# Performance work log

Hardware: AMD Instinct MI355X
Metric: run time of the kernel (lower is better)

Reference implementation:

```python
import jax, jax.numpy as jnp
import numpy as np
from jax import lax

T, B, DX, H, DZ = 512, 64, 128, 256, 64
W_SCALE = 0.05


def setup_inputs() -> dict:
    key = jax.random.key(0)
    ks = jax.random.split(key, 16)
    r = lambda k, shape, s=W_SCALE: jax.random.normal(k, shape, dtype=jnp.float32) * s
    return {
        "X": jax.random.normal(ks[0], (T, B, DX), dtype=jnp.float32),
        "Wih_f": r(ks[1], (H, DX)), "Whh_f": r(ks[2], (H, H)),
        "bih_f": r(ks[3], (H,)), "bhh_f": r(ks[4], (H,)),
        "Wih_b": r(ks[5], (H, DX)), "Whh_b": r(ks[6], (H, H)),
        "bih_b": r(ks[7], (H,)), "bhh_b": r(ks[8], (H,)),
        "Wt": r(ks[9], (H, DZ)), "bt": r(ks[10], (H,)),
        "Wmu": r(ks[11], (DZ, H)), "bmu": r(ks[12], (DZ,)),
        "Wsig": r(ks[13], (DZ, H)), "bsig": r(ks[14], (DZ,)),
        "eps": jax.random.normal(ks[15], (T, B, DZ), dtype=jnp.float32),
    }


def _rnn_dir(X, Wih, Whh, bih, bhh):
    # Elman RNN (tanh): h_t = tanh(x_t Wih^T + bih + h_{t-1} Whh^T + bhh)
    xproj = jnp.einsum('tbd,hd->tbh', X, Wih) + bih + bhh  # big GEMM hoisted out of scan

    def step(h, xp):
        h = jnp.tanh(xp + h @ Whh.T)
        return h, h

    h0 = jnp.zeros((X.shape[1], Whh.shape[0]), dtype=X.dtype)
    _, hs = lax.scan(step, h0, xproj)
    return hs  # [T,B,H]


def reference(X, Wih_f, Whh_f, bih_f, bhh_f, Wih_b, Whh_b, bih_b, bhh_b,
              Wt, bt, Wmu, bmu, Wsig, bsig, eps):
    h_left = _rnn_dir(X, Wih_f, Whh_f, bih_f, bhh_f)
    h_right = _rnn_dir(X[::-1], Wih_b, Whh_b, bih_b, bhh_b)[::-1]

    def step(z_prev, inputs):
        hl, hr, eps_t = inputs
        tmp = jnp.tanh(z_prev @ Wt.T + bt)           # transition_net
        h_t = (tmp + hl + hr) * (1.0 / 3.0)
        mu = h_t @ Wmu.T + bmu
        std = jax.nn.softplus(h_t @ Wsig.T + bsig)
        z = mu + std * eps_t                         # reparameterization
        return z, (z, mu, std)

    z0 = jnp.zeros((X.shape[1], Wt.shape[1]), dtype=X.dtype)
    _, (z, mu, std) = lax.scan(step, z0, (h_left, h_right, eps))
    # stack outputs {z_post, mu_post, std_post} into one array [3,T,B,DZ]
    return jnp.stack([z, mu, std])
```

## Files before the change

kernel.cpp:

```cpp
#include <hip/hip_runtime.h>

#define TT 512
#define BB 64
#define DXX 128
#define HH 256
#define DZZ 64

typedef __attribute__((ext_vector_type(8))) short short8;
typedef __attribute__((ext_vector_type(4))) float f32x4;

#define DEV static __device__ __forceinline__
#define MFMA(a,b,c) __builtin_amdgcn_mfma_f32_16x16x32_bf16((a),(b),(c),0,0,0)

DEV unsigned short f2bf(float f){
  unsigned u = __builtin_bit_cast(unsigned, f);
  u += 0x7FFFu + ((u >> 16) & 1u);
  return (unsigned short)(u >> 16);
}
DEV unsigned pack2(float lo, float hi){
  return (unsigned)f2bf(lo) | ((unsigned)f2bf(hi) << 16);
}
DEV float bfLO(unsigned u){ return __builtin_bit_cast(float, u << 16); }
DEV float bfHI(unsigned u){ return __builtin_bit_cast(float, u & 0xffff0000u); }
DEV float ftanh(float x){
  float a = fabsf(x);
  float e = __expf(-2.f * a);
  float r = __builtin_amdgcn_rcpf(1.f + e);
  float t = (1.f - e) * r;
  return copysignf(t, x);
}
DEV float fsoftplus(float x){
  float e = __expf(fminf(x, 20.f));
  float s = __logf(1.f + e);
  return (x > 20.f) ? x : s;
}
DEV void barrier_l(){
  asm volatile("s_waitcnt lgkmcnt(0)\n\ts_barrier" ::: "memory");
}


__global__ __launch_bounds__(256, 2) void phaseA(
    const float* __restrict__ X,
    const float* __restrict__ WihF, const float* __restrict__ bihF, const float* __restrict__ bhhF,
    const float* __restrict__ WihB, const float* __restrict__ bihB, const float* __restrict__ bhhB,
    unsigned short* __restrict__ xpF)
{
  const int bid = blockIdx.x;
  const int d = bid >> 9, s = bid & 511;
  const int ts = d ? (TT - 1 - s) : s;
  const float* W  = d ? WihB : WihF;
  const float* bi = d ? bihB : bihF;
  const float* bh = d ? bhhB : bhhF;

  const int tid = threadIdx.x, q = tid >> 6, l = tid & 63;
  const int l15 = l & 15, l4 = l >> 4;

  short8 wf[4][4];
  f32x4 bias[4];
  #pragma unroll
  for (int ni = 0; ni < 4; ++ni){
    int n = 64*q + 16*ni + l15;
    #pragma unroll
    for (int ks = 0; ks < 4; ++ks){
      const float* p = W + (size_t)n * DXX + ks*32 + l4*8;
      short8 v;
      #pragma unroll
      for (int i = 0; i < 8; ++i) v[i] = (short)f2bf(p[i]);
      wf[ni][ks] = v;
    }
    int n0 = 64*q + 16*ni + 4*l4;
    float4 b1 = *(const float4*)(bi + n0);
    float4 b2 = *(const float4*)(bh + n0);
    bias[ni][0]=b1.x+b2.x; bias[ni][1]=b1.y+b2.y; bias[ni][2]=b1.z+b2.z; bias[ni][3]=b1.w+b2.w;
  }

  #pragma unroll
  for (int bq = 0; bq < 4; ++bq){
    const float* xr = X + ((size_t)ts * 64 + 16*bq + l15) * DXX;
    short8 xf[4];
    #pragma unroll
    for (int ks = 0; ks < 4; ++ks){
      const float* p = xr + ks*32 + l4*8;
      short8 v;
      #pragma unroll
      for (int i = 0; i < 8; ++i) v[i] = (short)f2bf(p[i]);
      xf[ks] = v;
    }

    f32x4 acc[4];
    #pragma unroll
    for (int ni = 0; ni < 4; ++ni) acc[ni] = MFMA(wf[ni][0], xf[0], bias[ni]);
    #pragma unroll
    for (int ks = 1; ks < 4; ++ks)
      #pragma unroll
      for (int ni = 0; ni < 4; ++ni)
        acc[ni] = MFMA(wf[ni][ks], xf[ks], acc[ni]);

    unsigned wd[8];
    #pragma unroll
    for (int ni = 0; ni < 4; ++ni){
      wd[ni*2]   = pack2(acc[ni][0], acc[ni][1]);
      wd[ni*2+1] = pack2(acc[ni][2], acc[ni][3]);
    }
    unsigned short* dst = xpF + ((((size_t)d*TT + s)*4 + bq)*4 + q)*1024 + (size_t)l*16;
    uint4 o0 = {wd[0], wd[1], wd[2], wd[3]};
    uint4 o1 = {wd[4], wd[5], wd[6], wd[7]};
    ((uint4*)dst)[0] = o0;
    ((uint4*)dst)[1] = o1;
  }
}

__global__ __launch_bounds__(256, 1) void phaseB(
    const float* __restrict__ WhhF, const float* __restrict__ WhhB,
    const unsigned short* __restrict__ xpF, unsigned short* __restrict__ hF)
{
  const int dir = blockIdx.x >> 2, bq = blockIdx.x & 3;
  const float* Whh = dir ? WhhB : WhhF;
  const int tid = threadIdx.x, q = tid >> 6, l = tid & 63;
  const int l15 = l & 15, l4 = l >> 4;
  const int swz = (l15 & 7) << 3;
  const int rbase = l15 * 256;

  __shared__ __attribute__((aligned(16))) unsigned short hbuf[2][4096];

  short8 wf[4][8];
  #pragma unroll
  for (int ni = 0; ni < 4; ++ni){
    int n = 64*q + 16*ni + l15;
    #pragma unroll
    for (int ks = 0; ks < 8; ++ks){
      const float* p = Whh + (size_t)n * HH + ks*32 + l4*8;
      short8 v;
      #pragma unroll
      for (int i = 0; i < 8; ++i) v[i] = (short)f2bf(p[i]);
      wf[ni][ks] = v;
    }
  }
  for (int i = tid; i < 2048; i += 256) ((unsigned*)hbuf[0])[i] = 0u;

  const size_t strideS = 16384;
  const size_t laneOff = (size_t)bq*4096 + (size_t)q*1024 + (size_t)l*16;
  const unsigned short* xpP = xpF + (size_t)dir*TT*strideS + laneOff;
  unsigned short* hD = hF + (size_t)dir*TT*strideS + laneOff;

  uint4 xqA0, xqA1, xqB0, xqB1;
  { const uint4* p = (const uint4*)xpP;             xqA0 = p[0]; xqA1 = p[1]; }
  { const uint4* p = (const uint4*)(xpP + strideS); xqB0 = p[0]; xqB1 = p[1]; }

  barrier_l();

  auto bstep = [&](int s, uint4& XQ0, uint4& XQ1,
                   const unsigned short* RD, unsigned short* WR){
    short8 b[8];
    #pragma unroll
    for (int ks = 0; ks < 8; ++ks)
      b[ks] = *(const short8*)(RD + ((rbase + ks*32 + l4*8) ^ swz));
    f32x4 accE[4], accO[4];
    {
      unsigned W8[8] = {XQ0.x, XQ0.y, XQ0.z, XQ0.w, XQ1.x, XQ1.y, XQ1.z, XQ1.w};
      #pragma unroll
      for (int ni = 0; ni < 4; ++ni){
        accE[ni][0] = bfLO(W8[ni*2]);   accE[ni][1] = bfHI(W8[ni*2]);
        accE[ni][2] = bfLO(W8[ni*2+1]); accE[ni][3] = bfHI(W8[ni*2+1]);
        accO[ni][0] = 0.f; accO[ni][1] = 0.f; accO[ni][2] = 0.f; accO[ni][3] = 0.f;
      }
    }
    {
      int sn = (s + 2 < TT) ? s + 2 : TT - 1;
      const uint4* src = (const uint4*)(xpP + (size_t)sn * strideS);
      XQ0 = src[0]; XQ1 = src[1];
    }
    #pragma unroll
    for (int ks = 0; ks < 8; ks += 2){
      #pragma unroll
      for (int ni = 0; ni < 4; ++ni){
        accE[ni] = MFMA(wf[ni][ks],   b[ks],   accE[ni]);
        accO[ni] = MFMA(wf[ni][ks+1], b[ks+1], accO[ni]);
      }
    }
    unsigned wd[8];
    #pragma unroll
    for (int ni = 0; ni < 4; ++ni){
      float t0 = ftanh(accE[ni][0] + accO[ni][0]);
      float t1 = ftanh(accE[ni][1] + accO[ni][1]);
      float t2 = ftanh(accE[ni][2] + accO[ni][2]);
      float t3 = ftanh(accE[ni][3] + accO[ni][3]);
      unsigned lo = pack2(t0, t1), hi = pack2(t2, t3);
      wd[ni*2] = lo; wd[ni*2+1] = hi;
      int ea = rbase + ((64*q + 16*ni + 4*l4) ^ swz);
      uint2 v; v.x = lo; v.y = hi;
      *(uint2*)(WR + ea) = v;
    }
    {
      size_t off = (size_t)(dir ? (TT - 1 - s) : s) * strideS;
      uint4 o0 = {wd[0], wd[1], wd[2], wd[3]};
      uint4 o1 = {wd[4], wd[5], wd[6], wd[7]};
      *(uint4*)(hD + off)     = o0;
      *(uint4*)(hD + off + 8) = o1;
    }
    barrier_l();
  };

  for (int s = 0; s < TT; s += 2){
    bstep(s,     xqA0, xqA1, hbuf[0], hbuf[1]);
    bstep(s + 1, xqB0, xqB1, hbuf[1], hbuf[0]);
  }
}

__global__ __launch_bounds__(256, 1) void phaseC(
    const float* __restrict__ Wt,  const float* __restrict__ bt,
    const float* __restrict__ Wmu, const float* __restrict__ bmu,
    const float* __restrict__ Wsig,const float* __restrict__ bsig,
    const float* __restrict__ eps, const unsigned short* __restrict__ hF,
    float* __restrict__ out)
{
  const int bq = blockIdx.x;
  const int tid = threadIdx.x, q = tid >> 6, l = tid & 63;
  const int l15 = l & 15, l4 = l >> 4;
  const int swz = (l15 & 7) << 3;
  const int rbase = l15 * 256;
  const int zrbase = l15 * 64;

  __shared__ __attribute__((aligned(16))) unsigned short zbuf[1024];
  __shared__ __attribute__((aligned(16))) unsigned short hbuf[4096];

  short8 wtf[4][2]; f32x4 btb[4];
  #pragma unroll
  for (int ni = 0; ni < 4; ++ni){
    int n = 64*q + 16*ni + l15;
    #pragma unroll
    for (int ks = 0; ks < 2; ++ks){
      const float* p = Wt + (size_t)n * DZZ + ks*32 + l4*8;
      short8 v;
      #pragma unroll
      for (int i = 0; i < 8; ++i) v[i] = (short)f2bf(p[i]);
      wtf[ni][ks] = v;
    }
    float4 b4 = *(const float4*)(bt + 64*q + 16*ni + 4*l4);
    btb[ni][0]=b4.x; btb[ni][1]=b4.y; btb[ni][2]=b4.z; btb[ni][3]=b4.w;
  }
  short8 wm[8], wsg[8];
  {
    int r = 16*q + l15;
    #pragma unroll
    for (int ks = 0; ks < 8; ++ks){
      const float* pm = Wmu  + (size_t)r * HH + ks*32 + l4*8;
      const float* ps = Wsig + (size_t)r * HH + ks*32 + l4*8;
      short8 vm, vs;
      #pragma unroll
      for (int i = 0; i < 8; ++i){ vm[i] = (short)f2bf(pm[i]); vs[i] = (short)f2bf(ps[i]); }
      wm[ks] = vm; wsg[ks] = vs;
    }
  }
  f32x4 bm4, bs4;
  {
    float4 a = *(const float4*)(bmu  + 16*q + 4*l4);
    float4 b = *(const float4*)(bsig + 16*q + 4*l4);
    bm4[0]=a.x; bm4[1]=a.y; bm4[2]=a.z; bm4[3]=a.w;
    bs4[0]=b.x; bs4[1]=b.y; bs4[2]=b.z; bs4[3]=b.w;
  }
  for (int i = tid; i < 512; i += 256) ((unsigned*)zbuf)[i] = 0u;

  const size_t strideS = 16384;
  const size_t laneOff = (size_t)bq*4096 + (size_t)q*1024 + (size_t)l*16;
  const unsigned short* hLp = hF + laneOff;
  const unsigned short* hRp = hLp + (size_t)TT * strideS;
  const float* eP = eps + ((size_t)(16*bq + l15)) * 64 + 16*q + 4*l4;

  uint4 hlA0, hlA1, hrA0, hrA1, hlB0, hlB1, hrB0, hrB1;
  f32x4 efA, efB;
  {
    const uint4* sl = (const uint4*)hLp;              hlA0 = sl[0]; hlA1 = sl[1];
    const uint4* sr = (const uint4*)hRp;              hrA0 = sr[0]; hrA1 = sr[1];
    const uint4* tl = (const uint4*)(hLp + strideS);  hlB0 = tl[0]; hlB1 = tl[1];
    const uint4* tr = (const uint4*)(hRp + strideS);  hrB0 = tr[0]; hrB1 = tr[1];
    float4 e0 = *(const float4*)eP;
    float4 e1 = *(const float4*)(eP + 4096);
    efA[0]=e0.x; efA[1]=e0.y; efA[2]=e0.z; efA[3]=e0.w;
    efB[0]=e1.x; efB[1]=e1.y; efB[2]=e1.z; efB[3]=e1.w;
  }
  const size_t TBZ = (size_t)TT * 64 * 64;
  const f32x4 zero4 = {0.f, 0.f, 0.f, 0.f};
  barrier_l();

  auto cstep = [&](int t, uint4& HL0, uint4& HL1, uint4& HR0, uint4& HR1, f32x4& EF){
    short8 zb0 = *(const short8*)(zbuf + ((zrbase +  0 + l4*8) ^ swz));
    short8 zb1 = *(const short8*)(zbuf + ((zrbase + 32 + l4*8) ^ swz));
    f32x4 at[4];
    #pragma unroll
    for (int ni = 0; ni < 4; ++ni) at[ni] = MFMA(wtf[ni][0], zb0, btb[ni]);
    #pragma unroll
    for (int ni = 0; ni < 4; ++ni) at[ni] = MFMA(wtf[ni][1], zb1, at[ni]);
    {
      unsigned HLw[8] = {HL0.x, HL0.y, HL0.z, HL0.w, HL1.x, HL1.y, HL1.z, HL1.w};
      unsigned HRw[8] = {HR0.x, HR0.y, HR0.z, HR0.w, HR1.x, HR1.y, HR1.z, HR1.w};
      #pragma unroll
      for (int ni = 0; ni < 4; ++ni){
        unsigned wl0 = HLw[ni*2], wl1 = HLw[ni*2+1];
        unsigned wr0 = HRw[ni*2], wr1 = HRw[ni*2+1];
        float h0 = (ftanh(at[ni][0]) + bfLO(wl0) + bfLO(wr0)) * (1.f/3.f);
        float h1 = (ftanh(at[ni][1]) + bfHI(wl0) + bfHI(wr0)) * (1.f/3.f);
        float h2 = (ftanh(at[ni][2]) + bfLO(wl1) + bfLO(wr1)) * (1.f/3.f);
        float h3 = (ftanh(at[ni][3]) + bfHI(wl1) + bfHI(wr1)) * (1.f/3.f);
        int ea = rbase + ((64*q + 16*ni + 4*l4) ^ swz);
        uint2 v; v.x = pack2(h0, h1); v.y = pack2(h2, h3);
        *(uint2*)(hbuf + ea) = v;
      }
    }
    {
      int tn = (t + 2 < TT) ? t + 2 : TT - 1;
      const uint4* sl = (const uint4*)(hLp + (size_t)tn*strideS);
      const uint4* sr = (const uint4*)(hRp + (size_t)tn*strideS);
      HL0 = sl[0]; HL1 = sl[1]; HR0 = sr[0]; HR1 = sr[1];
    }
    barrier_l();

    short8 hb[8];
    #pragma unroll
    for (int ks = 0; ks < 8; ++ks)
      hb[ks] = *(const short8*)(hbuf + ((rbase + ks*32 + l4*8) ^ swz));
    f32x4 am0 = MFMA(wm[0],  hb[0], bm4);
    f32x4 as0 = MFMA(wsg[0], hb[0], bs4);
    f32x4 am1 = MFMA(wm[4],  hb[4], zero4);
    f32x4 as1 = MFMA(wsg[4], hb[4], zero4);
    #pragma unroll
    for (int ks = 1; ks < 4; ++ks){
      am0 = MFMA(wm[ks],    hb[ks],   am0);
      as0 = MFMA(wsg[ks],   hb[ks],   as0);
      am1 = MFMA(wm[ks+4],  hb[ks+4], am1);
      as1 = MFMA(wsg[ks+4], hb[ks+4], as1);
    }
    f32x4 mu = am0 + am1;
    f32x4 sg = as0 + as1;
    f32x4 dz, dsp;
    #pragma unroll
    for (int reg = 0; reg < 4; ++reg){
      float sp = fsoftplus(sg[reg]);
      dz[reg] = __builtin_fmaf(sp, EF[reg], mu[reg]);
      dsp[reg] = sp;
    }
    {
      int zea = zrbase + ((16*q + 4*l4) ^ swz);
      uint2 v; v.x = pack2(dz[0], dz[1]); v.y = pack2(dz[2], dz[3]);
      *(uint2*)(zbuf + zea) = v;
    }
    {
      int tn = (t + 2 < TT) ? t + 2 : TT - 1;
      float4 e4 = *(const float4*)(eP + (size_t)tn*4096);
      EF[0]=e4.x; EF[1]=e4.y; EF[2]=e4.z; EF[3]=e4.w;
    }
    {
      size_t ob = ((size_t)t*64 + 16*bq + l15)*64 + 16*q + 4*l4;
      *(float4*)(out + ob)         = *(float4*)&dz;
      *(float4*)(out + TBZ + ob)   = *(float4*)&mu;
      *(float4*)(out + 2*TBZ + ob) = *(float4*)&dsp;
    }
    barrier_l();
  };

  for (int t = 0; t < TT; t += 2){
    cstep(t,     hlA0, hlA1, hrA0, hrA1, efA);
    cstep(t + 1, hlB0, hlB1, hrB0, hrB1, efB);
  }
}

extern "C" void kernel_launch(void* const* d_in, const int* in_sizes, int n_in,
                              void* d_out, int out_size, void* d_ws, size_t ws_size,
                              hipStream_t stream)
{
  const float* X      = (const float*)d_in[0];
  const float* Wih_f  = (const float*)d_in[1];
  const float* Whh_f  = (const float*)d_in[2];
  const float* bih_f  = (const float*)d_in[3];
  const float* bhh_f  = (const float*)d_in[4];
  const float* Wih_b  = (const float*)d_in[5];
  const float* Whh_b  = (const float*)d_in[6];
  const float* bih_b  = (const float*)d_in[7];
  const float* bhh_b  = (const float*)d_in[8];
  const float* Wt     = (const float*)d_in[9];
  const float* bt     = (const float*)d_in[10];
  const float* Wmu    = (const float*)d_in[11];
  const float* bmu    = (const float*)d_in[12];
  const float* Wsig   = (const float*)d_in[13];
  const float* bsig   = (const float*)d_in[14];
  const float* eps    = (const float*)d_in[15];

  unsigned short* xpF = (unsigned short*)d_ws;
  unsigned short* hF  = xpF + (size_t)2 * TT * 16384;

  phaseA<<<dim3(1024), dim3(256), 0, stream>>>(X, Wih_f, bih_f, bhh_f, Wih_b, bih_b, bhh_b, xpF);
  phaseB<<<dim3(8), dim3(256), 0, stream>>>(Whh_f, Whh_b, xpF, hF);
  phaseC<<<dim3(4), dim3(256), 0, stream>>>(Wt, bt, Wmu, bmu, Wsig, bsig, eps, hF, (float*)d_out);
}
```

Baseline: 1.132 ms.

## Hoist hl+hr projection out of the z-scan and offload stores to helper waves

Because mu and sigma are linear in h_t, the contributions of h_left+h_right to them are precomputed in a new fully parallel phaseP kernel, with the 1/3 scale folded into the weights. The serial phaseC scan now only projects tanh(transition) through Wmu and Wsig each step. Both sequential kernels gain four extra waves that copy results from shared memory to global, one step behind, so the compute waves no longer issue global stores. This adds an extra kernel, an MS workspace buffer that reuses the xp region, and a slightly different bf16 rounding order.

```diff
diff --git a/kernel.cpp b/kernel.cpp
--- a/kernel.cpp
+++ b/kernel.cpp
@@ -1,7 +1,6 @@
 #include <hip/hip_runtime.h>
 
 #define TT 512
-#define BB 64
 #define DXX 128
 #define HH 256
 #define DZZ 64
@@ -86,7 +85,6 @@
       for (int i = 0; i < 8; ++i) v[i] = (short)f2bf(p[i]);
       xf[ks] = v;
     }
-
     f32x4 acc[4];
     #pragma unroll
     for (int ni = 0; ni < 4; ++ni) acc[ni] = MFMA(wf[ni][0], xf[0], bias[ni]);
@@ -110,135 +108,142 @@
   }
 }
 
-__global__ __launch_bounds__(256, 1) void phaseB(
+__global__ __launch_bounds__(512, 1) void phaseB(
     const float* __restrict__ WhhF, const float* __restrict__ WhhB,
     const unsigned short* __restrict__ xpF, unsigned short* __restrict__ hF)
 {
   const int dir = blockIdx.x >> 2, bq = blockIdx.x & 3;
   const float* Whh = dir ? WhhB : WhhF;
+  const int tid = threadIdx.x, w = tid >> 6, l = tid & 63;
+  const bool comp = (w < 4);
+  const int q = w & 3;
+  const int l15 = l & 15, l4 = l >> 4;
+  const int swz = (l15 & 7) << 3;
+  const int rbase = l15 * 256;
+
+  __shared__ __attribute__((aligned(16))) unsigned short hbuf[2][4096];
+  __shared__ __attribute__((aligned(16))) unsigned short hres[2][4096];
+
+  short8 wf[4][8];
+  if (comp){
+    #pragma unroll
+    for (int ni = 0; ni < 4; ++ni){
+      int n = 64*q + 16*ni + l15;
+      #pragma unroll
+      for (int ks = 0; ks < 8; ++ks){
+        const float* p = Whh + (size_t)n * HH + ks*32 + l4*8;
+        short8 v;
+        #pragma unroll
+        for (int i = 0; i < 8; ++i) v[i] = (short)f2bf(p[i]);
+        wf[ni][ks] = v;
+      }
+    }
+  }
+  for (int i = tid; i < 2048; i += 512) ((unsigned*)hbuf[0])[i] = 0u;
+
+  const size_t strideS = 16384;
+  const size_t laneOff = (size_t)bq*4096 + (size_t)q*1024 + (size_t)l*16;
+  const unsigned short* xpP = xpF + (size_t)dir*TT*strideS + laneOff;
+  unsigned short* hD = hF + (size_t)dir*TT*strideS + laneOff;
+
+  uint4 xqA0, xqA1, xqB0, xqB1;
+  if (comp){
+    const uint4* p0 = (const uint4*)xpP;             xqA0 = p0[0]; xqA1 = p0[1];
+    const uint4* p1 = (const uint4*)(xpP + strideS); xqB0 = p1[0]; xqB1 = p1[1];
+  }
+  __syncthreads();
+
+  auto bstep = [&](int s, uint4& XQ0, uint4& XQ1){
+    if (comp){
+      const unsigned short* RD = hbuf[s & 1];
+      unsigned short* WR = hbuf[(s & 1) ^ 1];
+      short8 b[8];
+      #pragma unroll
+      for (int ks = 0; ks < 8; ++ks)
+        b[ks] = *(const short8*)(RD + ((rbase + ks*32 + l4*8) ^ swz));
+      f32x4 accE[4], accO[4];
+      {
+        unsigned W8[8] = {XQ0.x, XQ0.y, XQ0.z, XQ0.w, XQ1.x, XQ1.y, XQ1.z, XQ1.w};
+        #pragma unroll
+        for (int ni = 0; ni < 4; ++ni){
+          accE[ni][0] = bfLO(W8[ni*2]);   accE[ni][1] = bfHI(W8[ni*2]);
+          accE[ni][2] = bfLO(W8[ni*2+1]); accE[ni][3] = bfHI(W8[ni*2+1]);
+          accO[ni][0] = 0.f; accO[ni][1] = 0.f; accO[ni][2] = 0.f; accO[ni][3] = 0.f;
+        }
+      }
+      {
+        int sn = (s + 2 < TT) ? s + 2 : TT - 1;
+        const uint4* src = (const uint4*)(xpP + (size_t)sn * strideS);
+        XQ0 = src[0]; XQ1 = src[1];
+      }
+      #pragma unroll
+      for (int ks = 0; ks < 8; ks += 2){
+        #pragma unroll
+        for (int ni = 0; ni < 4; ++ni){
+          accE[ni] = MFMA(wf[ni][ks],   b[ks],   accE[ni]);
+          accO[ni] = MFMA(wf[ni][ks+1], b[ks+1], accO[ni]);
+        }
+      }
+      unsigned wd[8];
+      #pragma unroll
+      for (int ni = 0; ni < 4; ++ni){
+        float t0 = ftanh(accE[ni][0] + accO[ni][0]);
+        float t1 = ftanh(accE[ni][1] + accO[ni][1]);
+        float t2 = ftanh(accE[ni][2] + accO[ni][2]);
+        float t3 = ftanh(accE[ni][3] + accO[ni][3]);
+        unsigned lo = pack2(t0, t1), hi = pack2(t2, t3);
+        wd[ni*2] = lo; wd[ni*2+1] = hi;
+        int ea = rbase + ((64*q + 16*ni + 4*l4) ^ swz);
+        uint2 v; v.x = lo; v.y = hi;
+        *(uint2*)(WR + ea) = v;
+      }
+      {
+        unsigned short* st = hres[s & 1] + q*1024 + l*16;
+        uint4 o0 = {wd[0], wd[1], wd[2], wd[3]};
+        uint4 o1 = {wd[4], wd[5], wd[6], wd[7]};
+        ((uint4*)st)[0] = o0;
+        ((uint4*)st)[1] = o1;
+      }
+    } else {
+      int sg = (s > 0) ? s - 1 : 0;
+      const unsigned short* src = hres[(s & 1) ^ 1] + q*1024 + l*16;
+      uint4 p0 = ((const uint4*)src)[0];
+      uint4 p1 = ((const uint4*)src)[1];
+      size_t off = (size_t)(dir ? (TT - 1 - sg) : sg) * strideS;
+      *(uint4*)(hD + off)     = p0;
+      *(uint4*)(hD + off + 8) = p1;
+    }
+    barrier_l();
+  };
+
+  for (int s = 0; s < TT; s += 2){
+    bstep(s,     xqA0, xqA1);
+    bstep(s + 1, xqB0, xqB1);
+  }
+  if (!comp){
+    const unsigned short* src = hres[1] + q*1024 + l*16;
+    uint4 p0 = ((const uint4*)src)[0];
+    uint4 p1 = ((const uint4*)src)[1];
+    size_t off = (size_t)(dir ? 0 : (TT - 1)) * strideS;
+    *(uint4*)(hD + off)     = p0;
+    *(uint4*)(hD + off + 8) = p1;
+  }
+}
+
+__global__ __launch_bounds__(256, 2) void phaseP(
+    const float* __restrict__ Wmu, const float* __restrict__ bmu,
+    const float* __restrict__ Wsig,const float* __restrict__ bsig,
+    const unsigned short* __restrict__ hF, float* __restrict__ MS)
+{
+  const int bid = blockIdx.x;
+  const int t = bid >> 2, bq = bid & 3;
   const int tid = threadIdx.x, q = tid >> 6, l = tid & 63;
   const int l15 = l & 15, l4 = l >> 4;
   const int swz = (l15 & 7) << 3;
   const int rbase = l15 * 256;
 
-  __shared__ __attribute__((aligned(16))) unsigned short hbuf[2][4096];
-
-  short8 wf[4][8];
-  #pragma unroll
-  for (int ni = 0; ni < 4; ++ni){
-    int n = 64*q + 16*ni + l15;
-    #pragma unroll
-    for (int ks = 0; ks < 8; ++ks){
-      const float* p = Whh + (size_t)n * HH + ks*32 + l4*8;
-      short8 v;
-      #pragma unroll
-      for (int i = 0; i < 8; ++i) v[i] = (short)f2bf(p[i]);
-      wf[ni][ks] = v;
-    }
-  }
-  for (int i = tid; i < 2048; i += 256) ((unsigned*)hbuf[0])[i] = 0u;
-
-  const size_t strideS = 16384;
-  const size_t laneOff = (size_t)bq*4096 + (size_t)q*1024 + (size_t)l*16;
-  const unsigned short* xpP = xpF + (size_t)dir*TT*strideS + laneOff;
-  unsigned short* hD = hF + (size_t)dir*TT*strideS + laneOff;
-
-  uint4 xqA0, xqA1, xqB0, xqB1;
-  { const uint4* p = (const uint4*)xpP;             xqA0 = p[0]; xqA1 = p[1]; }
-  { const uint4* p = (const uint4*)(xpP + strideS); xqB0 = p[0]; xqB1 = p[1]; }
-
-  barrier_l();
-
-  auto bstep = [&](int s, uint4& XQ0, uint4& XQ1,
-                   const unsigned short* RD, unsigned short* WR){
-    short8 b[8];
-    #pragma unroll
-    for (int ks = 0; ks < 8; ++ks)
-      b[ks] = *(const short8*)(RD + ((rbase + ks*32 + l4*8) ^ swz));
-    f32x4 accE[4], accO[4];
-    {
-      unsigned W8[8] = {XQ0.x, XQ0.y, XQ0.z, XQ0.w, XQ1.x, XQ1.y, XQ1.z, XQ1.w};
-      #pragma unroll
-      for (int ni = 0; ni < 4; ++ni){
-        accE[ni][0] = bfLO(W8[ni*2]);   accE[ni][1] = bfHI(W8[ni*2]);
-        accE[ni][2] = bfLO(W8[ni*2+1]); accE[ni][3] = bfHI(W8[ni*2+1]);
-        accO[ni][0] = 0.f; accO[ni][1] = 0.f; accO[ni][2] = 0.f; accO[ni][3] = 0.f;
-      }
-    }
-    {
-      int sn = (s + 2 < TT) ? s + 2 : TT - 1;
-      const uint4* src = (const uint4*)(xpP + (size_t)sn * strideS);
-      XQ0 = src[0]; XQ1 = src[1];
-    }
-    #pragma unroll
-    for (int ks = 0; ks < 8; ks += 2){
-      #pragma unroll
-      for (int ni = 0; ni < 4; ++ni){
-        accE[ni] = MFMA(wf[ni][ks],   b[ks],   accE[ni]);
-        accO[ni] = MFMA(wf[ni][ks+1], b[ks+1], accO[ni]);
-      }
-    }
-    unsigned wd[8];
-    #pragma unroll
-    for (int ni = 0; ni < 4; ++ni){
-      float t0 = ftanh(accE[ni][0] + accO[ni][0]);
-      float t1 = ftanh(accE[ni][1] + accO[ni][1]);
-      float t2 = ftanh(accE[ni][2] + accO[ni][2]);
-      float t3 = ftanh(accE[ni][3] + accO[ni][3]);
-      unsigned lo = pack2(t0, t1), hi = pack2(t2, t3);
-      wd[ni*2] = lo; wd[ni*2+1] = hi;
-      int ea = rbase + ((64*q + 16*ni + 4*l4) ^ swz);
-      uint2 v; v.x = lo; v.y = hi;
-      *(uint2*)(WR + ea) = v;
-    }
-    {
-      size_t off = (size_t)(dir ? (TT - 1 - s) : s) * strideS;
-      uint4 o0 = {wd[0], wd[1], wd[2], wd[3]};
-      uint4 o1 = {wd[4], wd[5], wd[6], wd[7]};
-      *(uint4*)(hD + off)     = o0;
-      *(uint4*)(hD + off + 8) = o1;
-    }
-    barrier_l();
-  };
-
-  for (int s = 0; s < TT; s += 2){
-    bstep(s,     xqA0, xqA1, hbuf[0], hbuf[1]);
-    bstep(s + 1, xqB0, xqB1, hbuf[1], hbuf[0]);
-  }
-}
-
-__global__ __launch_bounds__(256, 1) void phaseC(
-    const float* __restrict__ Wt,  const float* __restrict__ bt,
-    const float* __restrict__ Wmu, const float* __restrict__ bmu,
-    const float* __restrict__ Wsig,const float* __restrict__ bsig,
-    const float* __restrict__ eps, const unsigned short* __restrict__ hF,
-    float* __restrict__ out)
-{
-  const int bq = blockIdx.x;
-  const int tid = threadIdx.x, q = tid >> 6, l = tid & 63;
-  const int l15 = l & 15, l4 = l >> 4;
-  const int swz = (l15 & 7) << 3;
-  const int rbase = l15 * 256;
-  const int zrbase = l15 * 64;
-
-  __shared__ __attribute__((aligned(16))) unsigned short zbuf[1024];
   __shared__ __attribute__((aligned(16))) unsigned short hbuf[4096];
 
-  short8 wtf[4][2]; f32x4 btb[4];
-  #pragma unroll
-  for (int ni = 0; ni < 4; ++ni){
-    int n = 64*q + 16*ni + l15;
-    #pragma unroll
-    for (int ks = 0; ks < 2; ++ks){
-      const float* p = Wt + (size_t)n * DZZ + ks*32 + l4*8;
-      short8 v;
-      #pragma unroll
-      for (int i = 0; i < 8; ++i) v[i] = (short)f2bf(p[i]);
-      wtf[ni][ks] = v;
-    }
-    float4 b4 = *(const float4*)(bt + 64*q + 16*ni + 4*l4);
-    btb[ni][0]=b4.x; btb[ni][1]=b4.y; btb[ni][2]=b4.z; btb[ni][3]=b4.w;
-  }
   short8 wm[8], wsg[8];
   {
     int r = 16*q + l15;
@@ -248,7 +253,10 @@
       const float* ps = Wsig + (size_t)r * HH + ks*32 + l4*8;
       short8 vm, vs;
       #pragma unroll
-      for (int i = 0; i < 8; ++i){ vm[i] = (short)f2bf(pm[i]); vs[i] = (short)f2bf(ps[i]); }
+      for (int i = 0; i < 8; ++i){
+        vm[i] = (short)f2bf(pm[i] * (1.f/3.f));
+        vs[i] = (short)f2bf(ps[i] * (1.f/3.f));
+      }
       wm[ks] = vm; wsg[ks] = vs;
     }
   }
@@ -259,108 +267,217 @@
     bm4[0]=a.x; bm4[1]=a.y; bm4[2]=a.z; bm4[3]=a.w;
     bs4[0]=b.x; bs4[1]=b.y; bs4[2]=b.z; bs4[3]=b.w;
   }
-  for (int i = tid; i < 512; i += 256) ((unsigned*)zbuf)[i] = 0u;
 
   const size_t strideS = 16384;
   const size_t laneOff = (size_t)bq*4096 + (size_t)q*1024 + (size_t)l*16;
-  const unsigned short* hLp = hF + laneOff;
-  const unsigned short* hRp = hLp + (size_t)TT * strideS;
-  const float* eP = eps + ((size_t)(16*bq + l15)) * 64 + 16*q + 4*l4;
-
-  uint4 hlA0, hlA1, hrA0, hrA1, hlB0, hlB1, hrB0, hrB1;
-  f32x4 efA, efB;
+  const unsigned short* hl = hF + (size_t)t*strideS + laneOff;
+  const unsigned short* hr = hl + (size_t)TT*strideS;
   {
-    const uint4* sl = (const uint4*)hLp;              hlA0 = sl[0]; hlA1 = sl[1];
-    const uint4* sr = (const uint4*)hRp;              hrA0 = sr[0]; hrA1 = sr[1];
-    const uint4* tl = (const uint4*)(hLp + strideS);  hlB0 = tl[0]; hlB1 = tl[1];
-    const uint4* tr = (const uint4*)(hRp + strideS);  hrB0 = tr[0]; hrB1 = tr[1];
-    float4 e0 = *(const float4*)eP;
+    uint4 a0 = ((const uint4*)hl)[0], a1 = ((const uint4*)hl)[1];
+    uint4 b0 = ((const uint4*)hr)[0], b1 = ((const uint4*)hr)[1];
+    unsigned HL[8] = {a0.x,a0.y,a0.z,a0.w,a1.x,a1.y,a1.z,a1.w};
+    unsigned HR[8] = {b0.x,b0.y,b0.z,b0.w,b1.x,b1.y,b1.z,b1.w};
+    #pragma unroll
+    for (int ni = 0; ni < 4; ++ni){
+      float h0 = bfLO(HL[ni*2])   + bfLO(HR[ni*2]);
+      float h1 = bfHI(HL[ni*2])   + bfHI(HR[ni*2]);
+      float h2 = bfLO(HL[ni*2+1]) + bfLO(HR[ni*2+1]);
+      float h3 = bfHI(HL[ni*2+1]) + bfHI(HR[ni*2+1]);
+      int ea = rbase + ((64*q + 16*ni + 4*l4) ^ swz);
+      uint2 v; v.x = pack2(h0, h1); v.y = pack2(h2, h3);
+      *(uint2*)(hbuf + ea) = v;
+    }
+  }
+  __syncthreads();
+
+  short8 hb[8];
+  #pragma unroll
+  for (int ks = 0; ks < 8; ++ks)
+    hb[ks] = *(const short8*)(hbuf + ((rbase + ks*32 + l4*8) ^ swz));
+  const f32x4 zero4 = {0.f,0.f,0.f,0.f};
+  f32x4 am0 = MFMA(wm[0],  hb[0], bm4);
+  f32x4 as0 = MFMA(wsg[0], hb[0], bs4);
+  f32x4 am1 = MFMA(wm[4],  hb[4], zero4);
+  f32x4 as1 = MFMA(wsg[4], hb[4], zero4);
+  #pragma unroll
+  for (int ks = 1; ks < 4; ++ks){
+    am0 = MFMA(wm[ks],    hb[ks],   am0);
+    as0 = MFMA(wsg[ks],   hb[ks],   as0);
+    am1 = MFMA(wm[ks+4],  hb[ks+4], am1);
+    as1 = MFMA(wsg[ks+4], hb[ks+4], as1);
+  }
+  f32x4 mu = am0 + am1;
+  f32x4 sg = as0 + as1;
+  float* dst = MS + ((((size_t)t*4 + bq)*4 + q)*64 + (size_t)l)*8;
+  *(float4*)dst       = *(float4*)&mu;
+  *(float4*)(dst + 4) = *(float4*)&sg;
+}
+
+__global__ __launch_bounds__(512, 1) void phaseC(
+    const float* __restrict__ Wt,  const float* __restrict__ bt,
+    const float* __restrict__ Wmu, const float* __restrict__ Wsig,
+    const float* __restrict__ eps, const float* __restrict__ MS,
+    float* __restrict__ out)
+{
+  const int bq = blockIdx.x;
+  const int tid = threadIdx.x, w = tid >> 6, l = tid & 63;
+  const bool comp = (w < 4);
+  const int q = w & 3;
+  const int l15 = l & 15, l4 = l >> 4;
+  const int swz = (l15 & 7) << 3;
+  const int rbase = l15 * 256;
+  const int zrbase = l15 * 64;
+
+  __shared__ __attribute__((aligned(16))) unsigned short zbuf[1024];
+  __shared__ __attribute__((aligned(16))) unsigned short ubuf[4096];
+  __shared__ __attribute__((aligned(16))) float res[3072];
+
+  short8 wtf[4][2]; f32x4 btb[4];
+  short8 wm[8], wsg[8];
+  if (comp){
+    #pragma unroll
+    for (int ni = 0; ni < 4; ++ni){
+      int n = 64*q + 16*ni + l15;
+      #pragma unroll
+      for (int ks = 0; ks < 2; ++ks){
+        const float* p = Wt + (size_t)n * DZZ + ks*32 + l4*8;
+        short8 v;
+        #pragma unroll
+        for (int i = 0; i < 8; ++i) v[i] = (short)f2bf(p[i]);
+        wtf[ni][ks] = v;
+      }
+      float4 b4 = *(const float4*)(bt + 64*q + 16*ni + 4*l4);
+      btb[ni][0]=b4.x; btb[ni][1]=b4.y; btb[ni][2]=b4.z; btb[ni][3]=b4.w;
+    }
+    int r = 16*q + l15;
+    #pragma unroll
+    for (int ks = 0; ks < 8; ++ks){
+      const float* pm = Wmu  + (size_t)r * HH + ks*32 + l4*8;
+      const float* ps = Wsig + (size_t)r * HH + ks*32 + l4*8;
+      short8 vm, vs;
+      #pragma unroll
+      for (int i = 0; i < 8; ++i){
+        vm[i] = (short)f2bf(pm[i] * (1.f/3.f));
+        vs[i] = (short)f2bf(ps[i] * (1.f/3.f));
+      }
+      wm[ks] = vm; wsg[ks] = vs;
+    }
+  }
+  if (tid < 512) ((unsigned*)zbuf)[tid] = 0u;
+
+  const float* msP = MS + (((size_t)bq*4 + q)*64 + (size_t)l)*8;
+  const float* eP  = eps + ((size_t)(16*bq + l15))*64 + 16*q + 4*l4;
+  const int resoff = (q*64 + l)*12;
+  const size_t TBZ = (size_t)TT * 64 * 64;
+  const f32x4 zero4 = {0.f,0.f,0.f,0.f};
+
+  f32x4 MPa, SPa, EFa, MPb, SPb, EFb;
+  if (comp){
+    float4 m0 = *(const float4*)(msP);         float4 s0 = *(const float4*)(msP + 4);
+    float4 m1 = *(const float4*)(msP + 8192);  float4 s1 = *(const float4*)(msP + 8192 + 4);
+    float4 e0 = *(const float4*)(eP);
     float4 e1 = *(const float4*)(eP + 4096);
-    efA[0]=e0.x; efA[1]=e0.y; efA[2]=e0.z; efA[3]=e0.w;
-    efB[0]=e1.x; efB[1]=e1.y; efB[2]=e1.z; efB[3]=e1.w;
-  }
-  const size_t TBZ = (size_t)TT * 64 * 64;
-  const f32x4 zero4 = {0.f, 0.f, 0.f, 0.f};
-  barrier_l();
-
-  auto cstep = [&](int t, uint4& HL0, uint4& HL1, uint4& HR0, uint4& HR1, f32x4& EF){
-    short8 zb0 = *(const short8*)(zbuf + ((zrbase +  0 + l4*8) ^ swz));
-    short8 zb1 = *(const short8*)(zbuf + ((zrbase + 32 + l4*8) ^ swz));
-    f32x4 at[4];
-    #pragma unroll
-    for (int ni = 0; ni < 4; ++ni) at[ni] = MFMA(wtf[ni][0], zb0, btb[ni]);
-    #pragma unroll
-    for (int ni = 0; ni < 4; ++ni) at[ni] = MFMA(wtf[ni][1], zb1, at[ni]);
-    {
-      unsigned HLw[8] = {HL0.x, HL0.y, HL0.z, HL0.w, HL1.x, HL1.y, HL1.z, HL1.w};
-      unsigned HRw[8] = {HR0.x, HR0.y, HR0.z, HR0.w, HR1.x, HR1.y, HR1.z, HR1.w};
+    MPa[0]=m0.x;MPa[1]=m0.y;MPa[2]=m0.z;MPa[3]=m0.w;
+    SPa[0]=s0.x;SPa[1]=s0.y;SPa[2]=s0.z;SPa[3]=s0.w;
+    MPb[0]=m1.x;MPb[1]=m1.y;MPb[2]=m1.z;MPb[3]=m1.w;
+    SPb[0]=s1.x;SPb[1]=s1.y;SPb[2]=s1.z;SPb[3]=s1.w;
+    EFa[0]=e0.x;EFa[1]=e0.y;EFa[2]=e0.z;EFa[3]=e0.w;
+    EFb[0]=e1.x;EFb[1]=e1.y;EFb[2]=e1.z;EFb[3]=e1.w;
+  }
+  __syncthreads();
+
+  auto cstep = [&](int t, f32x4& MP, f32x4& SP, f32x4& EF){
+    if (comp){
+      short8 zb0 = *(const short8*)(zbuf + ((zrbase +  0 + l4*8) ^ swz));
+      short8 zb1 = *(const short8*)(zbuf + ((zrbase + 32 + l4*8) ^ swz));
+      f32x4 at[4];
+      #pragma unroll
+      for (int ni = 0; ni < 4; ++ni) at[ni] = MFMA(wtf[ni][0], zb0, btb[ni]);
+      #pragma unroll
+      for (int ni = 0; ni < 4; ++ni) at[ni] = MFMA(wtf[ni][1], zb1, at[ni]);
       #pragma unroll
       for (int ni = 0; ni < 4; ++ni){
-        unsigned wl0 = HLw[ni*2], wl1 = HLw[ni*2+1];
-        unsigned wr0 = HRw[ni*2], wr1 = HRw[ni*2+1];
-        float h0 = (ftanh(at[ni][0]) + bfLO(wl0) + bfLO(wr0)) * (1.f/3.f);
-        float h1 = (ftanh(at[ni][1]) + bfHI(wl0) + bfHI(wr0)) * (1.f/3.f);
-        float h2 = (ftanh(at[ni][2]) + bfLO(wl1) + bfLO(wr1)) * (1.f/3.f);
-        float h3 = (ftanh(at[ni][3]) + bfHI(wl1) + bfHI(wr1)) * (1.f/3.f);
+        float u0 = ftanh(at[ni][0]), u1 = ftanh(at[ni][1]);
+        float u2 = ftanh(at[ni][2]), u3 = ftanh(at[ni][3]);
         int ea = rbase + ((64*q + 16*ni + 4*l4) ^ swz);
-        uint2 v; v.x = pack2(h0, h1); v.y = pack2(h2, h3);
-        *(uint2*)(hbuf + ea) = v;
-      }
-    }
-    {
-      int tn = (t + 2 < TT) ? t + 2 : TT - 1;
-      const uint4* sl = (const uint4*)(hLp + (size_t)tn*strideS);
-      const uint4* sr = (const uint4*)(hRp + (size_t)tn*strideS);
-      HL0 = sl[0]; HL1 = sl[1]; HR0 = sr[0]; HR1 = sr[1];
+        uint2 v; v.x = pack2(u0, u1); v.y = pack2(u2, u3);
+        *(uint2*)(ubuf + ea) = v;
+      }
+    } else {
+      int tp = (t > 0) ? t - 1 : 0;
+      const float* rs = res + resoff;
+      float4 vz = *(const float4*)(rs);
+      float4 vm = *(const float4*)(rs + 4);
+      float4 vs = *(const float4*)(rs + 8);
+      size_t ob = ((size_t)tp*64 + 16*bq + l15)*64 + 16*q + 4*l4;
+      *(float4*)(out + ob)         = vz;
+      *(float4*)(out + TBZ + ob)   = vm;
+      *(float4*)(out + 2*TBZ + ob) = vs;
     }
     barrier_l();
 
-    short8 hb[8];
-    #pragma unroll
-    for (int ks = 0; ks < 8; ++ks)
-      hb[ks] = *(const short8*)(hbuf + ((rbase + ks*32 + l4*8) ^ swz));
-    f32x4 am0 = MFMA(wm[0],  hb[0], bm4);
-    f32x4 as0 = MFMA(wsg[0], hb[0], bs4);
-    f32x4 am1 = MFMA(wm[4],  hb[4], zero4);
-    f32x4 as1 = MFMA(wsg[4], hb[4], zero4);
-    #pragma unroll
-    for (int ks = 1; ks < 4; ++ks){
-      am0 = MFMA(wm[ks],    hb[ks],   am0);
-      as0 = MFMA(wsg[ks],   hb[ks],   as0);
-      am1 = MFMA(wm[ks+4],  hb[ks+4], am1);
-      as1 = MFMA(wsg[ks+4], hb[ks+4], as1);
-    }
-    f32x4 mu = am0 + am1;
-    f32x4 sg = as0 + as1;
-    f32x4 dz, dsp;
-    #pragma unroll
-    for (int reg = 0; reg < 4; ++reg){
-      float sp = fsoftplus(sg[reg]);
-      dz[reg] = __builtin_fmaf(sp, EF[reg], mu[reg]);
-      dsp[reg] = sp;
-    }
-    {
-      int zea = zrbase + ((16*q + 4*l4) ^ swz);
-      uint2 v; v.x = pack2(dz[0], dz[1]); v.y = pack2(dz[2], dz[3]);
-      *(uint2*)(zbuf + zea) = v;
-    }
-    {
-      int tn = (t + 2 < TT) ? t + 2 : TT - 1;
-      float4 e4 = *(const float4*)(eP + (size_t)tn*4096);
-      EF[0]=e4.x; EF[1]=e4.y; EF[2]=e4.z; EF[3]=e4.w;
-    }
-    {
-      size_t ob = ((size_t)t*64 + 16*bq + l15)*64 + 16*q + 4*l4;
-      *(float4*)(out + ob)         = *(float4*)&dz;
-      *(float4*)(out + TBZ + ob)   = *(float4*)&mu;
-      *(float4*)(out + 2*TBZ + ob) = *(float4*)&dsp;
+    if (comp){
+      short8 hb[8];
+      #pragma unroll
+      for (int ks = 0; ks < 8; ++ks)
+        hb[ks] = *(const short8*)(ubuf + ((rbase + ks*32 + l4*8) ^ swz));
+      f32x4 am0 = MFMA(wm[0],  hb[0], MP);
+      f32x4 as0 = MFMA(wsg[0], hb[0], SP);
+      f32x4 am1 = MFMA(wm[4],  hb[4], zero4);
+      f32x4 as1 = MFMA(wsg[4], hb[4], zero4);
+      #pragma unroll
+      for (int ks = 1; ks < 4; ++ks){
+        am0 = MFMA(wm[ks],    hb[ks],   am0);
+        as0 = MFMA(wsg[ks],   hb[ks],   as0);
+        am1 = MFMA(wm[ks+4],  hb[ks+4], am1);
+        as1 = MFMA(wsg[ks+4], hb[ks+4], as1);
+      }
+      f32x4 mu = am0 + am1;
+      f32x4 sg = as0 + as1;
+      f32x4 dz, dsp;
+      #pragma unroll
+      for (int reg = 0; reg < 4; ++reg){
+        float sp = fsoftplus(sg[reg]);
+        dz[reg] = __builtin_fmaf(sp, EF[reg], mu[reg]);
+        dsp[reg] = sp;
+      }
+      {
+        int zea = zrbase + ((16*q + 4*l4) ^ swz);
+        uint2 v; v.x = pack2(dz[0], dz[1]); v.y = pack2(dz[2], dz[3]);
+        *(uint2*)(zbuf + zea) = v;
+      }
+      {
+        float* rw = res + resoff;
+        *(float4*)(rw)     = *(float4*)&dz;
+        *(float4*)(rw + 4) = *(float4*)&mu;
+        *(float4*)(rw + 8) = *(float4*)&dsp;
+      }
+      {
+        int tn = (t + 2 < TT) ? t + 2 : TT - 1;
+        float4 m = *(const float4*)(msP + (size_t)tn*8192);
+        float4 s = *(const float4*)(msP + (size_t)tn*8192 + 4);
+        float4 e = *(const float4*)(eP + (size_t)tn*4096);
+        MP[0]=m.x;MP[1]=m.y;MP[2]=m.z;MP[3]=m.w;
+        SP[0]=s.x;SP[1]=s.y;SP[2]=s.z;SP[3]=s.w;
+        EF[0]=e.x;EF[1]=e.y;EF[2]=e.z;EF[3]=e.w;
+      }
     }
     barrier_l();
   };
 
   for (int t = 0; t < TT; t += 2){
-    cstep(t,     hlA0, hlA1, hrA0, hrA1, efA);
-    cstep(t + 1, hlB0, hlB1, hrB0, hrB1, efB);
+    cstep(t,     MPa, SPa, EFa);
+    cstep(t + 1, MPb, SPb, EFb);
+  }
+  if (!comp){
+    const float* rs = res + resoff;
+    float4 vz = *(const float4*)(rs);
+    float4 vm = *(const float4*)(rs + 4);
+    float4 vs = *(const float4*)(rs + 8);
+    size_t ob = ((size_t)(TT-1)*64 + 16*bq + l15)*64 + 16*q + 4*l4;
+    *(float4*)(out + ob)         = vz;
+    *(float4*)(out + TBZ + ob)   = vm;
+    *(float4*)(out + 2*TBZ + ob) = vs;
   }
 }
 
@@ -387,8 +504,10 @@
 
   unsigned short* xpF = (unsigned short*)d_ws;
   unsigned short* hF  = xpF + (size_t)2 * TT * 16384;
+  float* MS = (float*)d_ws;
 
   phaseA<<<dim3(1024), dim3(256), 0, stream>>>(X, Wih_f, bih_f, bhh_f, Wih_b, bih_b, bhh_b, xpF);
-  phaseB<<<dim3(8), dim3(256), 0, stream>>>(Whh_f, Whh_b, xpF, hF);
-  phaseC<<<dim3(4), dim3(256), 0, stream>>>(Wt, bt, Wmu, bmu, Wsig, bsig, eps, hF, (float*)d_out);
-}
+  phaseB<<<dim3(8), dim3(512), 0, stream>>>(Whh_f, Whh_b, xpF, hF);
+  phaseP<<<dim3(2048), dim3(256), 0, stream>>>(Wmu, bmu, Wsig, bsig, hF, MS);
+  phaseC<<<dim3(4), dim3(512), 0, stream>>>(Wt, bt, Wmu, Wsig, eps, MS, (float*)d_out);
+}
```

Result: slower. 1.155 ms (+2.0%).
